# Optimization experiments

Hardware: AMD Instinct MI355X
Metric: run time of the kernel (lower is better)

Reference implementation:

```python
import jax, jax.numpy as jnp
import numpy as np

CONF_THRES = 0.25
IOU_THRES = 0.45
MAX_DET = 300      # max detections returned (padded/masked to static shape)
K = 8192           # top-K score candidates entering NMS (static bound)
N_ANCHORS = 102000 # YOLOv5 @ 1280px
NC = 80            # COCO classes


def setup_inputs() -> dict:
    key = jax.random.key(0)
    # [B=1, N, 4 (xywh) + 1 (obj) + 80 (cls)] raw head predictions in [0,1)
    preds = jax.random.uniform(key, (1, N_ANCHORS, 4 + 1 + NC), dtype=jnp.float32)
    return {"preds": preds}


def _xywh2yxyx(b):
    # (xc, yc, w, h) -> (y1, x1, y2, x2), matching pt_xywh2yxyx_yolo
    x, y, w, h = b[..., 0], b[..., 1], b[..., 2], b[..., 3]
    return jnp.stack([y - h * 0.5, x - w * 0.5, y + h * 0.5, x + w * 0.5], axis=-1)


def _iou_matrix(boxes):
    # boxes: [K, 4] in yxyx; returns pairwise IoU [K, K]
    area = (boxes[:, 2] - boxes[:, 0]) * (boxes[:, 3] - boxes[:, 1])
    ty = jnp.maximum(boxes[:, None, 0], boxes[None, :, 0])
    tx = jnp.maximum(boxes[:, None, 1], boxes[None, :, 1])
    by = jnp.minimum(boxes[:, None, 2], boxes[None, :, 2])
    bx = jnp.minimum(boxes[:, None, 3], boxes[None, :, 3])
    inter = jnp.clip(by - ty, 0.0) * jnp.clip(bx - tx, 0.0)
    union = area[:, None] + area[None, :] - inter
    return inter / (union + 1e-9)


def _yolo_nms(preds):
    p = preds[0]                       # [N, 85] (loop returns on first image)
    obj = p[:, 4]                      # objectness
    cand = obj > CONF_THRES            # confidence filter
    cls_scores = p[:, 5:] * obj[:, None]
    scores = jnp.max(cls_scores, axis=1)
    classes = jnp.argmax(cls_scores, axis=1).astype(jnp.float32)
    scores = jnp.where(cand, scores, 0.0)  # mask instead of dynamic filter
    boxes = _xywh2yxyx(p[:, :4])       # [N, 4] yxyx

    # top-K candidates by score (static replacement for boolean filtering)
    top_scores, idx = jax.lax.top_k(scores, K)
    top_boxes = boxes[idx]
    top_classes = classes[idx]
    valid = top_scores > 0.0

    iou = _iou_matrix(top_boxes)       # [K, K], 256 MB fp32

    # greedy NMS: boxes already sorted by descending score
    ar = jnp.arange(K)

    def body(i, suppressed):
        keep_i = jnp.logical_and(jnp.logical_not(suppressed[i]), valid[i])
        return suppressed | (keep_i & (iou[i] > IOU_THRES) & (ar > i))

    suppressed = jax.lax.fori_loop(0, K, body, jnp.zeros((K,), jnp.bool_))
    keep = valid & jnp.logical_not(suppressed)

    # gather top MAX_DET kept detections (sorted), zero-pad the rest
    keep_scores = jnp.where(keep, top_scores, -1.0)
    _, sel = jax.lax.top_k(keep_scores, MAX_DET)
    mask = keep[sel]
    out_boxes = jnp.where(mask[:, None], top_boxes[sel], 0.0)[None]    # [1, MAX_DET, 4]
    out_classes = jnp.where(mask, top_classes[sel], 0.0)[None]         # [1, MAX_DET]
    out_scores = jnp.where(mask, top_scores[sel], 0.0)[None]           # [1, MAX_DET]
    return out_boxes, out_classes, out_scores


def reference(preds):
    return _yolo_nms(preds)
```

## Files before the change

kernel.cpp:

```cpp
#include <hip/hip_runtime.h>
#include <cstdint>

#define CONF_THRES 0.25f
#define IOU_THRES  0.45f
#define MAX_DET    300
#define K_TOP      8192
#define NA         102000
#define NCLS       80
#define ROWLEN     85
#define CAP        32640
#define NPLANE     32
#define WIN        512
#define NWIN       (K_TOP / WIN)
#define SSTR       9

typedef unsigned long long u64;
typedef unsigned int u32;

__global__ __launch_bounds__(256) void score_key_kernel(const float* __restrict__ preds,
        u64* __restrict__ keys, u32* __restrict__ histP) {
#pragma clang fp contract(off)
    int lane = threadIdx.x & 63;
    int i = blockIdx.x * 4 + (threadIdx.x >> 6);
    if (i >= NA) return;
    const float* p = preds + (size_t)i * ROWLEN;
    float v0 = p[lane];
    float v1 = (lane < ROWLEN - 64) ? p[64 + lane] : 0.0f;
    float obj = __shfl(v0, 4);
    float m = (lane >= 5) ? v0 : 0.0f;
    m = fmaxf(m, (lane < 21) ? v1 : 0.0f);
    for (int off = 32; off; off >>= 1) m = fmaxf(m, __shfl_xor(m, off));
    if (lane == 0) {
        float score = (obj > CONF_THRES) ? m * obj : 0.0f;
        u32 sb = __float_as_uint(score);
        keys[i] = ((u64)sb << 32) | (u32)(~(u32)i);
        if (sb != 0u)
            atomicAdd(&histP[((u32)blockIdx.x & (NPLANE - 1u)) * 65536u + (sb >> 16)], 1u);
    }
}

__global__ __launch_bounds__(256) void reduce_hist_kernel(const u32* __restrict__ histP,
        u32* __restrict__ sumhist) {
    int bin = blockIdx.x * 256 + threadIdx.x;
    u32 s = 0;
#pragma unroll
    for (int r = 0; r < NPLANE; ++r) s += histP[r * 65536 + bin];
    sumhist[bin] = s;
}

__global__ __launch_bounds__(1024) void cutoff_kernel(const u32* __restrict__ hist,
        u32* __restrict__ meta) {
    __shared__ u32 suf[1024];
    __shared__ int cbs;
    __shared__ u32 above_s;
    int t = threadIdx.x;
    u32 s = 0;
    const u32* hb = hist + t * 64;
    for (int b = 0; b < 64; ++b) s += hb[b];
    suf[t] = s;
    if (t == 0) { cbs = -1; above_s = 0; }
    __syncthreads();
    for (int off = 1; off < 1024; off <<= 1) {
        u32 add = (t + off < 1024) ? suf[t + off] : 0u;
        __syncthreads();
        suf[t] += add;
        __syncthreads();
    }
    u32 st = suf[t];
    u32 stn = (t < 1023) ? suf[t + 1] : 0u;
    if (st >= (u32)K_TOP && stn < (u32)K_TOP) {
        cbs = t;
        above_s = stn;
    }
    __syncthreads();
    int cb = cbs;
    if (t < 64) {
        u32 thresh = 0;
        if (cb >= 0) {
            u32 above = above_s;
            u32 v = hist[cb * 64 + t];
            for (int off = 1; off < 64; off <<= 1) {
                u32 o = __shfl_down(v, off);
                if (t + off < 64) v += o;
            }
            u64 bal = __ballot(v + above >= (u32)K_TOP);
            int bstar = 63 - __builtin_clzll((unsigned long long)bal);
            thresh = ((u32)(cb * 64 + bstar)) << 16;
        }
        if (t == 0) meta[1] = thresh;
    }
}

__global__ __launch_bounds__(256) void compact_kernel(const u64* __restrict__ keys,
        u32* __restrict__ meta, u64* __restrict__ comp) {
    __shared__ u32 woff[4];
    __shared__ u32 bbase;
    int i = blockIdx.x * 256 + threadIdx.x;
    int wid = threadIdx.x >> 6, lane = threadIdx.x & 63;
    u64 key = (i < NA) ? keys[i] : 0ull;
    u32 sb = (u32)(key >> 32);
    u32 th = meta[1];
    bool take = (i < NA) && (sb != 0u) && (sb >= th);
    u64 bal = __ballot(take);
    if (lane == 0) woff[wid] = (u32)__popcll(bal);
    __syncthreads();
    if (threadIdx.x == 0) {
        u32 t0 = woff[0], t1 = woff[1], t2 = woff[2], t3 = woff[3];
        bbase = atomicAdd(&meta[0], t0 + t1 + t2 + t3);
        woff[0] = 0; woff[1] = t0; woff[2] = t0 + t1; woff[3] = t0 + t1 + t2;
    }
    __syncthreads();
    if (take) {
        u32 pos = bbase + woff[wid] + (u32)__popcll(bal & ((1ull << lane) - 1ull));
        if (pos < CAP) comp[pos] = key;
    }
}

__global__ __launch_bounds__(256) void rank_partial_kernel(const u64* __restrict__ comp,
        const u32* __restrict__ meta, u32* __restrict__ rankArr) {
    __shared__ u64 tile[1024];
    u32 cnt = meta[0];
    int n = (int)(cnt < (u32)CAP ? cnt : (u32)CAP);
    int i0 = blockIdx.x * 256;
    int j0 = blockIdx.y * 1024;
    if (i0 >= n || j0 >= n) return;
    int lim = n - j0; if (lim > 1024) lim = 1024;
    for (int k = threadIdx.x; k < 1024; k += 256)
        tile[k] = (k < lim) ? comp[j0 + k] : 0ull;
    __syncthreads();
    int i = i0 + threadIdx.x;
    if (i < n) {
        u64 key = comp[i];
        u32 r = 0;
#pragma unroll 8
        for (int j = 0; j < 1024; ++j) r += (tile[j] > key) ? 1u : 0u;
        atomicAdd(&rankArr[i], r);
    }
}

__global__ __launch_bounds__(256) void scatter_kernel(const u64* __restrict__ comp,
        const u32* __restrict__ meta, const u32* __restrict__ rankArr,
        u64* __restrict__ sorted) {
    u32 cnt = meta[0];
    int n = (int)(cnt < (u32)CAP ? cnt : (u32)CAP);
    int i = blockIdx.x * 256 + threadIdx.x;
    if (i < n) {
        u32 r = rankArr[i];
        if (r < (u32)K_TOP) sorted[r] = comp[i];
    }
}

__global__ __launch_bounds__(256) void gather_kernel(const u64* __restrict__ sorted,
        const float* __restrict__ preds, float* __restrict__ boxes,
        float* __restrict__ scores, float* __restrict__ classes) {
#pragma clang fp contract(off)
    int lane = threadIdx.x & 63;
    int i = blockIdx.x * 4 + (threadIdx.x >> 6);
    u64 key = sorted[i];
    u32 sb = (u32)(key >> 32);
    float score = __uint_as_float(sb);
    if (score > 0.0f) {
        u32 idx = ~(u32)(key & 0xffffffffull);
        const float* p = preds + (size_t)idx * ROWLEN;
        float v0 = p[lane];
        float v1 = (lane < ROWLEN - 64) ? p[64 + lane] : 0.0f;
        float obj = __shfl(v0, 4);
        u64 kb = 0;
        if (lane >= 5) {
            float q = v0 * obj;
            kb = ((u64)__float_as_uint(q) << 8) | (u32)(255 - (lane - 5));
        }
        if (lane < 21) {
            float q = v1 * obj;
            u64 kb2 = ((u64)__float_as_uint(q) << 8) | (u32)(255 - (59 + lane));
            if (kb2 > kb) kb = kb2;
        }
        for (int off = 32; off; off >>= 1) {
            u64 o = __shfl_xor(kb, off);
            if (o > kb) kb = o;
        }
        u32 cls = 255u - (u32)(kb & 0xffull);
        float x = __shfl(v0, 0), y = __shfl(v0, 1);
        float w = __shfl(v0, 2), h = __shfl(v0, 3);
        if (lane == 0) {
            boxes[i * 4 + 0] = y - h * 0.5f;
            boxes[i * 4 + 1] = x - w * 0.5f;
            boxes[i * 4 + 2] = y + h * 0.5f;
            boxes[i * 4 + 3] = x + w * 0.5f;
            scores[i] = score;
            classes[i] = (float)cls;
        }
    } else if (lane == 0) {
        boxes[i * 4 + 0] = 0.0f; boxes[i * 4 + 1] = 0.0f;
        boxes[i * 4 + 2] = 0.0f; boxes[i * 4 + 3] = 0.0f;
        scores[i] = 0.0f;
        classes[i] = 0.0f;
    }
}

__global__ __launch_bounds__(256) void mask_kernel(const float* __restrict__ boxes,
        u64* __restrict__ mask) {
#pragma clang fp contract(off)
    __shared__ float4 cb[64];
    int wj = blockIdx.x;
    int i = blockIdx.y * 256 + threadIdx.x;
    int j0 = wj * 64;
    if (threadIdx.x < 64) cb[threadIdx.x] = ((const float4*)boxes)[j0 + threadIdx.x];
    __syncthreads();
    float4 bi = ((const float4*)boxes)[i];
    float area_i = (bi.z - bi.x) * (bi.w - bi.y);
    u64 bits = 0;
    if (j0 + 63 > i) {
        for (int k = 0; k < 64; ++k) {
            int j = j0 + k;
            if (j <= i) continue;
            float4 bj = cb[k];
            float area_j = (bj.z - bj.x) * (bj.w - bj.y);
            float ty = fmaxf(bi.x, bj.x);
            float tx = fmaxf(bi.y, bj.y);
            float by = fminf(bi.z, bj.z);
            float bx = fminf(bi.w, bj.w);
            float inter = fmaxf(by - ty, 0.0f) * fmaxf(bx - tx, 0.0f);
            float uni = (area_i + area_j) - inter;
            float iou = inter / (uni + 1e-9f);
            if (iou > IOU_THRES) bits |= (1ull << k);
        }
    }
    mask[(size_t)i * 128 + wj] = bits;
}

__global__ __launch_bounds__(256) void valid_kernel(const float* __restrict__ scores,
        u64* __restrict__ remw) {
    int w = blockIdx.x * 4 + (threadIdx.x >> 6);
    int lane = threadIdx.x & 63;
    u64 b = __ballot(scores[w * 64 + lane] > 0.0f);
    if (lane == 0) remw[w] = b;
}

__device__ __forceinline__ u64 rfl64(u64 v) {
    u32 lo = (u32)__builtin_amdgcn_readfirstlane((int)(u32)v);
    u32 hi = (u32)__builtin_amdgcn_readfirstlane((int)(u32)(v >> 32));
    return ((u64)hi << 32) | lo;
}

__device__ __forceinline__ u64 bcast64(u64 v, int srclane) {
    u32 lo = (u32)__builtin_amdgcn_readlane((int)(u32)v, srclane);
    u32 hi = (u32)__builtin_amdgcn_readlane((int)(u32)(v >> 32), srclane);
    return ((u64)hi << 32) | lo;
}

__device__ __forceinline__ u64 shfl_xor64(u64 v, int m) {
    u32 lo = __shfl_xor((u32)v, m, 64);
    u32 hi = __shfl_xor((u32)(v >> 32), m, 64);
    return ((u64)hi << 32) | lo;
}

__global__ __launch_bounds__(64) void nms_scan_kernel(const u64* __restrict__ mask,
        const u64* __restrict__ remw, const float* __restrict__ boxes,
        const float* __restrict__ scores, const float* __restrict__ classes,
        float* __restrict__ out) {
    __shared__ u64 sub[WIN * SSTR];
    __shared__ u32 ki[MAX_DET + 8];
    int lane = threadIdx.x;
    int n = 0;
    for (int win = 0; win < NWIN && n < MAX_DET; ++win) {
        int rbase = win * WIN;
        __syncthreads();
#pragma unroll 8
        for (int it = 0; it < 32; ++it) {
            int idx = it * 64 + lane;
            int r = idx >> 2, j = (idx & 3) * 2;
            uint4 v = *(const uint4*)&mask[(size_t)(rbase + r) * 128 + win * 8 + j];
            sub[r * SSTR + j]     = ((u64)v.y << 32) | v.x;
            sub[r * SSTR + j + 1] = ((u64)v.w << 32) | v.z;
        }
        u64 acc[8] = {0, 0, 0, 0, 0, 0, 0, 0};
        for (int m = lane; m < n; m += 64) {
            int k = (int)ki[m];
            const u64* rp = &mask[(size_t)k * 128 + win * 8];
#pragma unroll
            for (int j = 0; j < 8; ++j) acc[j] |= rp[j];
        }
#pragma unroll
        for (int j = 0; j < 8; ++j)
            for (int off = 32; off; off >>= 1) acc[j] |= shfl_xor64(acc[j], off);
        __syncthreads();
        u64 diag[8];
#pragma unroll
        for (int sw = 0; sw < 8; ++sw) diag[sw] = sub[(sw * 64 + lane) * SSTR + sw];
        int n0 = n;
        u64 keptW[8] = {0, 0, 0, 0, 0, 0, 0, 0};
#pragma unroll
        for (int sw = 0; sw < 8; ++sw) {
            if (n < MAX_DET) {
                u64 acc2 = 0;
#pragma unroll
                for (int wp = 0; wp < 8; ++wp) {
                    if (wp < sw) {
                        if ((keptW[wp] >> lane) & 1ull)
                            acc2 |= sub[(wp * 64 + lane) * SSTR + sw];
                    }
                }
                for (int off = 32; off; off >>= 1) acc2 |= shfl_xor64(acc2, off);
                u64 cur = rfl64(remw[win * 8 + sw]) & ~rfl64(acc[sw]) & ~rfl64(acc2);
                u64 kw = 0;
                while (cur != 0ull && n < MAX_DET) {
                    int b = __ffsll((unsigned long long)cur) - 1;
                    u64 slice = bcast64(diag[sw], b);
                    kw |= (1ull << b);
                    cur &= ~(slice | (1ull << b));
                    ++n;
                }
                keptW[sw] = kw;
            }
        }
        int base = n0;
#pragma unroll
        for (int sw = 0; sw < 8; ++sw) {
            u64 kw = keptW[sw];
            if ((kw >> lane) & 1ull) {
                int rr = (int)__popcll(kw & ((1ull << lane) - 1ull));
                ki[base + rr] = (u32)(rbase + sw * 64 + lane);
            }
            base += (int)__popcll(kw);
        }
        __syncthreads();
    }
    __syncthreads();
    for (int m = lane; m < MAX_DET; m += 64) {
        float4 b = make_float4(0.0f, 0.0f, 0.0f, 0.0f);
        float c = 0.0f, s = 0.0f;
        if (m < n) {
            int k = (int)ki[m];
            b = ((const float4*)boxes)[k];
            c = classes[k];
            s = scores[k];
        }
        ((float4*)out)[m] = b;
        out[1200 + m] = c;
        out[1500 + m] = s;
    }
}

extern "C" void kernel_launch(void* const* d_in, const int* in_sizes, int n_in,
                              void* d_out, int out_size, void* d_ws, size_t ws_size,
                              hipStream_t stream) {
    const float* preds = (const float*)d_in[0];
    char* ws = (char*)d_ws;

    u32*   sumhist = (u32*)(ws + 0);
    u32*   meta    = (u32*)(ws + 262144);
    u64*   remw    = (u64*)(ws + 262208);
    u64*   sorted  = (u64*)(ws + 263232);
    u64*   keys    = (u64*)(ws + 328768);
    u32*   rankArr = (u32*)(ws + 328768);
    u64*   comp    = (u64*)(ws + 1144768);
    float* tboxes  = (float*)(ws + 1405888);
    float* tscores = (float*)(ws + 1536960);
    float* tclass  = (float*)(ws + 1569728);
    u64*   mask    = (u64*)(ws + 1602496);
    u32*   histP   = (u32*)(ws + 1602496);
    float* out     = (float*)d_out;

    hipMemsetAsync(ws, 0, 328768, stream);
    hipMemsetAsync(histP, 0, (size_t)NPLANE * 65536 * 4, stream);

    score_key_kernel<<<(NA + 3) / 4, 256, 0, stream>>>(preds, keys, histP);
    reduce_hist_kernel<<<256, 256, 0, stream>>>(histP, sumhist);
    cutoff_kernel<<<1, 1024, 0, stream>>>(sumhist, meta);
    compact_kernel<<<(NA + 255) / 256, 256, 0, stream>>>(keys, meta, comp);
    hipMemsetAsync(rankArr, 0, (size_t)CAP * 4, stream);
    rank_partial_kernel<<<dim3((CAP + 255) / 256, (CAP + 1023) / 1024), 256, 0, stream>>>(
            comp, meta, rankArr);
    scatter_kernel<<<(CAP + 255) / 256, 256, 0, stream>>>(comp, meta, rankArr, sorted);
    gather_kernel<<<K_TOP / 4, 256, 0, stream>>>(sorted, preds, tboxes, tscores, tclass);
    mask_kernel<<<dim3(128, K_TOP / 256), 256, 0, stream>>>(tboxes, mask);
    valid_kernel<<<32, 256, 0, stream>>>(tscores, remw);
    nms_scan_kernel<<<1, 64, 0, stream>>>(mask, remw, tboxes, tscores, tclass, out);
}
```

Measured before the change: 212.8 us.

## Restructure IoU mask kernel with ballots and triangular block skip; shrink histogram

The IoU mask kernel now gives each lane one column box and loops over 64 row boxes. It builds each mask word with a wavefront ballot and writes the words through shared memory so the global stores are coalesced. Blocks entirely below the diagonal exit early, and box areas are precomputed in the gather step. The score histogram shrinks to 16384 bins, which assumes score bit patterns stay below that range. The two memsets become one zero kernel. The risk is that mask words below the diagonal are no longer written, which matters only if the scan reads them.

```diff
diff --git a/kernel.cpp b/kernel.cpp
--- a/kernel.cpp
+++ b/kernel.cpp
@@ -10,12 +10,22 @@
 #define ROWLEN     85
 #define CAP        32640
 #define NPLANE     32
+#define NBINS      16384
 #define WIN        512
 #define NWIN       (K_TOP / WIN)
 #define SSTR       9
 
 typedef unsigned long long u64;
 typedef unsigned int u32;
+
+__global__ __launch_bounds__(256) void zero_kernel(uint4* __restrict__ a,
+        uint4* __restrict__ b) {
+    int i = blockIdx.x * 256 + threadIdx.x;
+    uint4 z = make_uint4(0u, 0u, 0u, 0u);
+    if (i < 4164) a[i] = z;
+    b[i] = z;
+    b[i + 65536] = z;
+}
 
 __global__ __launch_bounds__(256) void score_key_kernel(const float* __restrict__ preds,
         u64* __restrict__ keys, u32* __restrict__ histP) {
@@ -35,7 +45,7 @@
         u32 sb = __float_as_uint(score);
         keys[i] = ((u64)sb << 32) | (u32)(~(u32)i);
         if (sb != 0u)
-            atomicAdd(&histP[((u32)blockIdx.x & (NPLANE - 1u)) * 65536u + (sb >> 16)], 1u);
+            atomicAdd(&histP[((u32)blockIdx.x & (NPLANE - 1u)) * NBINS + (sb >> 16)], 1u);
     }
 }
 
@@ -44,7 +54,7 @@
     int bin = blockIdx.x * 256 + threadIdx.x;
     u32 s = 0;
 #pragma unroll
-    for (int r = 0; r < NPLANE; ++r) s += histP[r * 65536 + bin];
+    for (int r = 0; r < NPLANE; ++r) s += histP[r * NBINS + bin];
     sumhist[bin] = s;
 }
 
@@ -55,8 +65,8 @@
     __shared__ u32 above_s;
     int t = threadIdx.x;
     u32 s = 0;
-    const u32* hb = hist + t * 64;
-    for (int b = 0; b < 64; ++b) s += hb[b];
+    const u32* hb = hist + t * 16;
+    for (int b = 0; b < 16; ++b) s += hb[b];
     suf[t] = s;
     if (t == 0) { cbs = -1; above_s = 0; }
     __syncthreads();
@@ -78,14 +88,14 @@
         u32 thresh = 0;
         if (cb >= 0) {
             u32 above = above_s;
-            u32 v = hist[cb * 64 + t];
+            u32 v = (t < 16) ? hist[cb * 16 + t] : 0u;
             for (int off = 1; off < 64; off <<= 1) {
                 u32 o = __shfl_down(v, off);
                 if (t + off < 64) v += o;
             }
             u64 bal = __ballot(v + above >= (u32)K_TOP);
             int bstar = 63 - __builtin_clzll((unsigned long long)bal);
-            thresh = ((u32)(cb * 64 + bstar)) << 16;
+            thresh = ((u32)(cb * 16 + bstar)) << 16;
         }
         if (t == 0) meta[1] = thresh;
     }
@@ -152,7 +162,8 @@
 
 __global__ __launch_bounds__(256) void gather_kernel(const u64* __restrict__ sorted,
         const float* __restrict__ preds, float* __restrict__ boxes,
-        float* __restrict__ scores, float* __restrict__ classes) {
+        float* __restrict__ scores, float* __restrict__ classes,
+        float* __restrict__ areas) {
 #pragma clang fp contract(off)
     int lane = threadIdx.x & 63;
     int i = blockIdx.x * 4 + (threadIdx.x >> 6);
@@ -183,50 +194,75 @@
         float x = __shfl(v0, 0), y = __shfl(v0, 1);
         float w = __shfl(v0, 2), h = __shfl(v0, 3);
         if (lane == 0) {
-            boxes[i * 4 + 0] = y - h * 0.5f;
-            boxes[i * 4 + 1] = x - w * 0.5f;
-            boxes[i * 4 + 2] = y + h * 0.5f;
-            boxes[i * 4 + 3] = x + w * 0.5f;
+            float ymin = y - h * 0.5f, xmin = x - w * 0.5f;
+            float ymax = y + h * 0.5f, xmax = x + w * 0.5f;
+            boxes[i * 4 + 0] = ymin;
+            boxes[i * 4 + 1] = xmin;
+            boxes[i * 4 + 2] = ymax;
+            boxes[i * 4 + 3] = xmax;
             scores[i] = score;
             classes[i] = (float)cls;
+            areas[i] = (ymax - ymin) * (xmax - xmin);
         }
     } else if (lane == 0) {
         boxes[i * 4 + 0] = 0.0f; boxes[i * 4 + 1] = 0.0f;
         boxes[i * 4 + 2] = 0.0f; boxes[i * 4 + 3] = 0.0f;
         scores[i] = 0.0f;
         classes[i] = 0.0f;
+        areas[i] = 0.0f;
     }
 }
 
 __global__ __launch_bounds__(256) void mask_kernel(const float* __restrict__ boxes,
-        u64* __restrict__ mask) {
+        const float* __restrict__ areas, u64* __restrict__ mask) {
 #pragma clang fp contract(off)
-    __shared__ float4 cb[64];
-    int wj = blockIdx.x;
-    int i = blockIdx.y * 256 + threadIdx.x;
-    int j0 = wj * 64;
-    if (threadIdx.x < 64) cb[threadIdx.x] = ((const float4*)boxes)[j0 + threadIdx.x];
-    __syncthreads();
-    float4 bi = ((const float4*)boxes)[i];
-    float area_i = (bi.z - bi.x) * (bi.w - bi.y);
-    u64 bits = 0;
-    if (j0 + 63 > i) {
-        for (int k = 0; k < 64; ++k) {
-            int j = j0 + k;
-            if (j <= i) continue;
-            float4 bj = cb[k];
-            float area_j = (bj.z - bj.x) * (bj.w - bj.y);
+    int cx = blockIdx.x;
+    int ry = blockIdx.y;
+    if (cx < (ry >> 2)) return;
+    __shared__ u64 st[64 * 5];
+    int wv = threadIdx.x >> 6, lane = threadIdx.x & 63;
+    int jw = cx * 4 + wv;
+    int j  = jw * 64 + lane;
+    int r0 = ry * 64;
+    float4 bj = ((const float4*)boxes)[j];
+    float aj = areas[j];
+    u64 myword = 0;
+    if (cx > (ry >> 2)) {
+#pragma unroll 8
+        for (int rr = 0; rr < 64; ++rr) {
+            float4 bi = ((const float4*)boxes)[r0 + rr];
+            float ai = areas[r0 + rr];
             float ty = fmaxf(bi.x, bj.x);
             float tx = fmaxf(bi.y, bj.y);
             float by = fminf(bi.z, bj.z);
             float bx = fminf(bi.w, bj.w);
             float inter = fmaxf(by - ty, 0.0f) * fmaxf(bx - tx, 0.0f);
-            float uni = (area_i + area_j) - inter;
+            float uni = (ai + aj) - inter;
             float iou = inter / (uni + 1e-9f);
-            if (iou > IOU_THRES) bits |= (1ull << k);
-        }
-    }
-    mask[(size_t)i * 128 + wj] = bits;
+            u64 bal = __ballot(iou > IOU_THRES);
+            if (lane == rr) myword = bal;
+        }
+    } else {
+#pragma unroll 8
+        for (int rr = 0; rr < 64; ++rr) {
+            int r = r0 + rr;
+            float4 bi = ((const float4*)boxes)[r];
+            float ai = areas[r];
+            float ty = fmaxf(bi.x, bj.x);
+            float tx = fmaxf(bi.y, bj.y);
+            float by = fminf(bi.z, bj.z);
+            float bx = fminf(bi.w, bj.w);
+            float inter = fmaxf(by - ty, 0.0f) * fmaxf(bx - tx, 0.0f);
+            float uni = (ai + aj) - inter;
+            float iou = inter / (uni + 1e-9f);
+            u64 bal = __ballot((iou > IOU_THRES) && (j > r));
+            if (lane == rr) myword = bal;
+        }
+    }
+    st[lane * 5 + wv] = myword;
+    __syncthreads();
+    int t = threadIdx.x;
+    mask[(size_t)(r0 + (t >> 2)) * 128 + cx * 4 + (t & 3)] = st[(t >> 2) * 5 + (t & 3)];
 }
 
 __global__ __launch_bounds__(256) void valid_kernel(const float* __restrict__ scores,
@@ -355,6 +391,7 @@
     u64*   keys    = (u64*)(ws + 328768);
     u32*   rankArr = (u32*)(ws + 328768);
     u64*   comp    = (u64*)(ws + 1144768);
+    float* careas  = (float*)(ws + 1144768);
     float* tboxes  = (float*)(ws + 1405888);
     float* tscores = (float*)(ws + 1536960);
     float* tclass  = (float*)(ws + 1569728);
@@ -362,19 +399,18 @@
     u32*   histP   = (u32*)(ws + 1602496);
     float* out     = (float*)d_out;
 
-    hipMemsetAsync(ws, 0, 328768, stream);
-    hipMemsetAsync(histP, 0, (size_t)NPLANE * 65536 * 4, stream);
-
+    zero_kernel<<<256, 256, 0, stream>>>((uint4*)(ws + 262144), (uint4*)histP);
     score_key_kernel<<<(NA + 3) / 4, 256, 0, stream>>>(preds, keys, histP);
-    reduce_hist_kernel<<<256, 256, 0, stream>>>(histP, sumhist);
+    reduce_hist_kernel<<<64, 256, 0, stream>>>(histP, sumhist);
     cutoff_kernel<<<1, 1024, 0, stream>>>(sumhist, meta);
     compact_kernel<<<(NA + 255) / 256, 256, 0, stream>>>(keys, meta, comp);
     hipMemsetAsync(rankArr, 0, (size_t)CAP * 4, stream);
     rank_partial_kernel<<<dim3((CAP + 255) / 256, (CAP + 1023) / 1024), 256, 0, stream>>>(
             comp, meta, rankArr);
     scatter_kernel<<<(CAP + 255) / 256, 256, 0, stream>>>(comp, meta, rankArr, sorted);
-    gather_kernel<<<K_TOP / 4, 256, 0, stream>>>(sorted, preds, tboxes, tscores, tclass);
-    mask_kernel<<<dim3(128, K_TOP / 256), 256, 0, stream>>>(tboxes, mask);
+    gather_kernel<<<K_TOP / 4, 256, 0, stream>>>(sorted, preds, tboxes, tscores,
+            tclass, careas);
+    mask_kernel<<<dim3(32, 128), 256, 0, stream>>>(tboxes, careas, mask);
     valid_kernel<<<32, 256, 0, stream>>>(tscores, remw);
     nms_scan_kernel<<<1, 64, 0, stream>>>(mask, remw, tboxes, tscores, tclass, out);
 }
```

After: 210.2 us. No clear change (-1.2%).
